# Kernel tuning notes

Measured on AMD Instinct MI355X. Metric: run time of the kernel, lower is better.

The kernel has to match this reference:

```python
import jax, jax.numpy as jnp
import numpy as np

B, NH, T, D = 2, 16, 2048, 64

def setup_inputs() -> dict:
    key = jax.random.key(0)
    kq, kk, kv = jax.random.split(key, 3)
    Q = jax.random.normal(kq, (B, NH, T, D), dtype=jnp.float32)
    K = jax.random.normal(kk, (B, NH, T, D), dtype=jnp.float32)
    V = jax.random.normal(kv, (B, NH, T, D), dtype=jnp.float32)
    return {"Q": Q, "K": K, "V": V}

def reference(Q, K, V):
    # scores: [B, nh, T, T]
    Dh = Q.shape[-1]
    scale = 1.0 / jnp.sqrt(jnp.asarray(Dh, Q.dtype))
    scores = jnp.einsum('bhtd,bhsd->bhts', Q, K) * scale
    Tq = Q.shape[2]
    causal = jnp.tril(jnp.ones((Tq, Tq), dtype=bool))
    scores = jnp.where(causal, scores, jnp.asarray(-jnp.inf, scores.dtype))
    attn = jax.nn.softmax(scores, axis=-1)
    return jnp.einsum('bhts,bhsd->bhtd', attn, V)
```

## Files before the change

kernel.cpp:

```cpp
#include <hip/hip_runtime.h>
#include <hip/hip_bf16.h>


typedef __bf16 bf16;
typedef __bf16 bf16x2 __attribute__((ext_vector_type(2)));
typedef __bf16 bf16x4 __attribute__((ext_vector_type(4)));
typedef __bf16 bf16x8 __attribute__((ext_vector_type(8)));
typedef float floatx4 __attribute__((ext_vector_type(4)));

#define T_SEQ 2048
#define DH 64
#define TKS 32
#define BHN 32
#define CEXP 0.18033688011112042f

__device__ __forceinline__ void gload16(const bf16* g, bf16* l) {
    __builtin_amdgcn_global_load_lds(
        (const __attribute__((address_space(1))) void*)g,
        (__attribute__((address_space(3))) void*)l, 16, 0, 0);
}

__global__ __launch_bounds__(256) void prep(const float* __restrict__ K,
                                            const float* __restrict__ V,
                                            bf16* __restrict__ Kb,
                                            bf16* __restrict__ Vt) {
    const int bid = (int)blockIdx.x;
    const int tid = (int)threadIdx.x;
    if (bid < 512) {
        size_t i = ((size_t)bid * 256 + tid) * 8;
        #pragma unroll
        for (int it = 0; it < 4; ++it) {
            float4 a = *(const float4*)(K + i + 0);
            float4 b = *(const float4*)(K + i + 4);
            bf16x8 o;
            o[0]=(bf16)(a.x*CEXP); o[1]=(bf16)(a.y*CEXP); o[2]=(bf16)(a.z*CEXP); o[3]=(bf16)(a.w*CEXP);
            o[4]=(bf16)(b.x*CEXP); o[5]=(bf16)(b.y*CEXP); o[6]=(bf16)(b.z*CEXP); o[7]=(bf16)(b.w*CEXP);
            *(bf16x8*)(Kb + i) = o;
            i += (size_t)512 * 256 * 8;
        }
        return;
    }
    __shared__ bf16 tile[2][64][72];
    const int vb = bid - 512;
    const int bh = vb & (BHN - 1);
    const int tp = (vb >> 5) * 128;
    #pragma unroll
    for (int tt = 0; tt < 2; ++tt) {
        const int r = tid >> 2;
        const int c = (tid & 3) * 16;
        const float* s = V + ((size_t)bh * T_SEQ + tp + tt * 64 + r) * DH + c;
        float4 f0 = *(const float4*)(s + 0);
        float4 f1 = *(const float4*)(s + 4);
        float4 f2 = *(const float4*)(s + 8);
        float4 f3 = *(const float4*)(s + 12);
        bf16x8 p0, p1;
        p0[0]=(bf16)f0.x; p0[1]=(bf16)f0.y; p0[2]=(bf16)f0.z; p0[3]=(bf16)f0.w;
        p0[4]=(bf16)f1.x; p0[5]=(bf16)f1.y; p0[6]=(bf16)f1.z; p0[7]=(bf16)f1.w;
        p1[0]=(bf16)f2.x; p1[1]=(bf16)f2.y; p1[2]=(bf16)f2.z; p1[3]=(bf16)f2.w;
        p1[4]=(bf16)f3.x; p1[5]=(bf16)f3.y; p1[6]=(bf16)f3.z; p1[7]=(bf16)f3.w;
        *(bf16x8*)&tile[tt][r][c + 0] = p0;
        *(bf16x8*)&tile[tt][r][c + 8] = p1;
    }
    __syncthreads();
    #pragma unroll
    for (int tt = 0; tt < 2; ++tt) {
        const int d   = tid >> 2;
        const int tch = (tid & 3) * 16;
        bf16x8 o0, o1;
        #pragma unroll
        for (int j = 0; j < 8; ++j) { o0[j] = tile[tt][tch + j][d]; o1[j] = tile[tt][tch + 8 + j][d]; }
        bf16* o = Vt + ((size_t)bh * DH + d) * T_SEQ + tp + tt * 64 + tch;
        *(bf16x8*)(o + 0) = o0;
        *(bf16x8*)(o + 8) = o1;
    }
}

__global__ __launch_bounds__(256, 3)
void fa_fwd(const float* __restrict__ Qg, const bf16* __restrict__ Kb,
            const bf16* __restrict__ Vt, float* __restrict__ Og)
{
    __shared__ __align__(16) bf16 smem[24576];

    const int gid   = (int)blockIdx.x;
    const int jt    = 31 - (gid >> 5);
    const int bh    = gid & (BHN - 1);

    const int tid  = (int)threadIdx.x;
    const int wave = tid >> 6;
    const int lane = tid & 63;
    const int quad = lane >> 4;
    const int l16  = lane & 15;
    const int psw  = (l16 >> 1) & 3;

    const int hf = wave >> 1;
    const int sp = wave & 1;

    const int qbaseW = jt * 64 + hf * 32;
    const int ntileW = 2 * jt + 1 + hf;
    const int c0  = (ntileW + 1) >> 1;
    const int tw0 = sp ? c0 : 0;
    const int tw1 = sp ? ntileW : c0;
    const int cnt = tw1 - tw0;

    bf16* W = smem + wave * 6144;

    const bf16* Kbh = Kb + (size_t)bh * (T_SEQ * DH);
    const bf16* Vbh = Vt + (size_t)bh * (DH * T_SEQ);
    const size_t qrb = (size_t)bh * T_SEQ;

    const int rl  = lane >> 3;
    const int kch = (lane & 7) ^ (rl & 7);
    const int vr  = lane >> 2;
    const int vch = (lane & 3) ^ ((lane >> 3) & 3);

    floatx4 oacc[4][2];
    #pragma unroll
    for (int mt = 0; mt < 4; ++mt)
        #pragma unroll
        for (int nt = 0; nt < 2; ++nt) oacc[mt][nt] = (floatx4){0.f,0.f,0.f,0.f};
    float lpart[2] = {0.f, 0.f};

    auto stageK = [&](int kt, bf16* dst) {
        const bf16* kg = Kbh + (size_t)kt * TKS * DH;
        #pragma unroll
        for (int g = 0; g < 4; ++g)
            gload16(kg + (size_t)(g * 8 + rl) * DH + kch * 8, dst + g * 512);
    };
    auto stageV = [&](int kt, bf16* dst) {
        const bf16* vg = Vbh + kt * TKS;
        #pragma unroll
        for (int g = 0; g < 4; ++g)
            gload16(vg + (size_t)(g * 16 + vr) * T_SEQ + vch * 8, dst + g * 512);
    };

    auto pk2 = [&](float a, float b) -> unsigned {
        bf16x2 h; h[0] = (bf16)a; h[1] = (bf16)b;
        return __builtin_bit_cast(unsigned, h);
    };

    if (cnt > 0) {
        bf16x8 qb[2][2];
        #pragma unroll
        for (int nt = 0; nt < 2; ++nt) {
            const int qrow = qbaseW + nt * 16 + l16;
            #pragma unroll
            for (int kk = 0; kk < 2; ++kk) {
                const float* s = Qg + (qrb + qrow) * DH + kk * 32 + quad * 8;
                float4 f0 = *(const float4*)(s);
                float4 f1 = *(const float4*)(s + 4);
                bf16x8 t;
                t[0]=(bf16)f0.x; t[1]=(bf16)f0.y; t[2]=(bf16)f0.z; t[3]=(bf16)f0.w;
                t[4]=(bf16)f1.x; t[5]=(bf16)f1.y; t[6]=(bf16)f1.z; t[7]=(bf16)f1.w;
                qb[nt][kk] = t;
            }
        }

        stageK(tw0, W);
        stageV(tw0, W + 4096);

        for (int t = tw0; t < tw1; ++t) {
            const int cur = (t - tw0) & 1;
            bf16* Kcur = W + cur * 2048;
            bf16* Vcur = W + 4096;
            const int k0 = t * TKS;

            const bool pf = (t + 1 < tw1);
            if (pf) {
                stageK(t + 1, W + (cur ^ 1) * 2048);
                __builtin_amdgcn_s_waitcnt(0x0F78);
            } else {
                __builtin_amdgcn_s_waitcnt(0x0F70);
            }

            floatx4 sa[2][2];
            #pragma unroll
            for (int mt = 0; mt < 2; ++mt)
                #pragma unroll
                for (int nt = 0; nt < 2; ++nt) sa[mt][nt] = (floatx4){0.f,0.f,0.f,0.f};
            __builtin_amdgcn_s_setprio(1);
            #pragma unroll
            for (int kk = 0; kk < 2; ++kk) {
                #pragma unroll
                for (int mt = 0; mt < 2; ++mt) {
                    bf16x8 kf = *(const bf16x8*)&Kcur[(mt * 16 + l16) * 64 + (((kk * 4 + quad) ^ (l16 & 7)) * 8)];
                    #pragma unroll
                    for (int nt = 0; nt < 2; ++nt)
                        sa[mt][nt] = __builtin_amdgcn_mfma_f32_16x16x32_bf16(kf, qb[nt][kk], sa[mt][nt], 0, 0, 0);
                }
            }
            __builtin_amdgcn_s_setprio(0);
            if (k0 + TKS - 1 > qbaseW) {
                #pragma unroll
                for (int mt = 0; mt < 2; ++mt)
                    #pragma unroll
                    for (int nt = 0; nt < 2; ++nt) {
                        const int qg = qbaseW + nt * 16 + l16;
                        #pragma unroll
                        for (int r = 0; r < 4; ++r) {
                            const int keyg = k0 + mt * 16 + quad * 4 + r;
                            if (keyg > qg) sa[mt][nt][r] = -INFINITY;
                        }
                    }
            }
            bf16x8 pfr[2];
            #pragma unroll
            for (int nt = 0; nt < 2; ++nt) {
                float p0[4], p1[4];
                #pragma unroll
                for (int r = 0; r < 4; ++r) {
                    p0[r] = __builtin_amdgcn_exp2f(sa[0][nt][r]);
                    p1[r] = __builtin_amdgcn_exp2f(sa[1][nt][r]);
                    lpart[nt] += p0[r] + p1[r];
                }
                unsigned X0 = pk2(p0[0], p0[1]);
                unsigned X1 = pk2(p0[2], p0[3]);
                unsigned Y0 = pk2(p1[0], p1[1]);
                unsigned Y1 = pk2(p1[2], p1[3]);
                asm("v_permlane32_swap_b32 %0, %1" : "+v"(X0), "+v"(Y0));
                asm("v_permlane16_swap_b32 %0, %1" : "+v"(X0), "+v"(Y0));
                asm("v_permlane32_swap_b32 %0, %1" : "+v"(X1), "+v"(Y1));
                asm("v_permlane16_swap_b32 %0, %1" : "+v"(X1), "+v"(Y1));
                uint4 u; u.x = X0; u.y = X1; u.z = Y0; u.w = Y1;
                pfr[nt] = __builtin_bit_cast(bf16x8, u);
            }
            if (pf) __builtin_amdgcn_s_waitcnt(0x0F74);
            bf16x8 vf[4];
            #pragma unroll
            for (int mt = 0; mt < 4; ++mt)
                vf[mt] = *(const bf16x8*)&Vcur[(mt * 16 + l16) * 32 + ((quad ^ psw) * 8)];
            if (pf) {
                __builtin_amdgcn_s_waitcnt(0xC07F);
                stageV(t + 1, Vcur);
            }
            __builtin_amdgcn_s_setprio(1);
            #pragma unroll
            for (int mt = 0; mt < 4; ++mt) {
                #pragma unroll
                for (int nt = 0; nt < 2; ++nt)
                    oacc[mt][nt] = __builtin_amdgcn_mfma_f32_16x16x32_bf16(vf[mt], pfr[nt], oacc[mt][nt], 0, 0, 0);
            }
            __builtin_amdgcn_s_setprio(0);
        }
    }

    __syncthreads();
    if (sp == 1) {
        bf16* a = smem + hf * 4608;
        float* al = (float*)(a + 4096);
        #pragma unroll
        for (int f = 0; f < 8; ++f) {
            bf16x4 w;
            #pragma unroll
            for (int e = 0; e < 4; ++e) w[e] = (bf16)oacc[f >> 1][f & 1][e];
            *(bf16x4*)&a[(f * 64 + lane) * 4] = w;
        }
        #pragma unroll
        for (int nt = 0; nt < 2; ++nt)
            al[nt * 64 + lane] = lpart[nt];
    }
    __syncthreads();
    if (sp == 0) {
        const bf16* a = smem + hf * 4608;
        const float* al = (const float*)(a + 4096);
        #pragma unroll
        for (int f = 0; f < 8; ++f) {
            bf16x4 w = *(const bf16x4*)&a[(f * 64 + lane) * 4];
            #pragma unroll
            for (int e = 0; e < 4; ++e) oacc[f >> 1][f & 1][e] += (float)w[e];
        }
        #pragma unroll
        for (int nt = 0; nt < 2; ++nt) lpart[nt] += al[nt * 64 + lane];

        float invl[2];
        #pragma unroll
        for (int nt = 0; nt < 2; ++nt) {
            float v = lpart[nt];
            v += __shfl_xor(v, 16);
            v += __shfl_xor(v, 32);
            invl[nt] = 1.0f / v;
        }
        #pragma unroll
        for (int nt = 0; nt < 2; ++nt) {
            const size_t qrow = qrb + qbaseW + nt * 16 + l16;
            #pragma unroll
            for (int mt = 0; mt < 4; ++mt) {
                float4 o;
                o.x = oacc[mt][nt][0] * invl[nt];
                o.y = oacc[mt][nt][1] * invl[nt];
                o.z = oacc[mt][nt][2] * invl[nt];
                o.w = oacc[mt][nt][3] * invl[nt];
                *(float4*)&Og[qrow * DH + mt * 16 + quad * 4] = o;
            }
        }
    }
}

extern "C" void kernel_launch(void* const* d_in, const int* in_sizes, int n_in,
                              void* d_out, int out_size, void* d_ws, size_t ws_size,
                              hipStream_t stream) {
    const float* Q = (const float*)d_in[0];
    const float* K = (const float*)d_in[1];
    const float* V = (const float*)d_in[2];
    float* O = (float*)d_out;
    (void)in_sizes; (void)n_in; (void)out_size; (void)ws_size;

    const size_t nelem = (size_t)BHN * T_SEQ * DH;
    bf16* Kbf = (bf16*)d_ws;
    bf16* Vtb = Kbf + nelem;

    prep<<<dim3(1024), dim3(256), 0, stream>>>(K, V, Kbf, Vtb);
    fa_fwd<<<dim3(1024), dim3(256), 0, stream>>>(Q, Kbf, Vtb, O);
}
```

Baseline: 127.6 us.

## Share K/V tiles across waves with block-wide double buffering

```diff
diff --git a/kernel.cpp b/kernel.cpp
--- a/kernel.cpp
+++ b/kernel.cpp
@@ -75,15 +75,16 @@
     }
 }
 
-__global__ __launch_bounds__(256, 3)
+__global__ __launch_bounds__(256, 4)
 void fa_fwd(const float* __restrict__ Qg, const bf16* __restrict__ Kb,
             const bf16* __restrict__ Vt, float* __restrict__ Og)
 {
-    __shared__ __align__(16) bf16 smem[24576];
-
-    const int gid   = (int)blockIdx.x;
-    const int jt    = 31 - (gid >> 5);
-    const int bh    = gid & (BHN - 1);
+    __shared__ __align__(16) bf16 smem[8192];
+
+    const int gid    = (int)blockIdx.x;
+    const int jt     = gid >> 5;
+    const int bh     = gid & (BHN - 1);
+    const int ntiles = 2 * jt + 2;
 
     const int tid  = (int)threadIdx.x;
     const int wave = tid >> 6;
@@ -92,17 +93,7 @@
     const int l16  = lane & 15;
     const int psw  = (l16 >> 1) & 3;
 
-    const int hf = wave >> 1;
-    const int sp = wave & 1;
-
-    const int qbaseW = jt * 64 + hf * 32;
-    const int ntileW = 2 * jt + 1 + hf;
-    const int c0  = (ntileW + 1) >> 1;
-    const int tw0 = sp ? c0 : 0;
-    const int tw1 = sp ? ntileW : c0;
-    const int cnt = tw1 - tw0;
-
-    bf16* W = smem + wave * 6144;
+    const int qw0 = jt * 64 + wave * 16;
 
     const bf16* Kbh = Kb + (size_t)bh * (T_SEQ * DH);
     const bf16* Vbh = Vt + (size_t)bh * (DH * T_SEQ);
@@ -112,25 +103,14 @@
     const int kch = (lane & 7) ^ (rl & 7);
     const int vr  = lane >> 2;
     const int vch = (lane & 3) ^ ((lane >> 3) & 3);
-
-    floatx4 oacc[4][2];
-    #pragma unroll
-    for (int mt = 0; mt < 4; ++mt)
-        #pragma unroll
-        for (int nt = 0; nt < 2; ++nt) oacc[mt][nt] = (floatx4){0.f,0.f,0.f,0.f};
-    float lpart[2] = {0.f, 0.f};
-
-    auto stageK = [&](int kt, bf16* dst) {
-        const bf16* kg = Kbh + (size_t)kt * TKS * DH;
-        #pragma unroll
-        for (int g = 0; g < 4; ++g)
-            gload16(kg + (size_t)(g * 8 + rl) * DH + kch * 8, dst + g * 512);
-    };
-    auto stageV = [&](int kt, bf16* dst) {
-        const bf16* vg = Vbh + kt * TKS;
-        #pragma unroll
-        for (int g = 0; g < 4; ++g)
-            gload16(vg + (size_t)(g * 16 + vr) * T_SEQ + vch * 8, dst + g * 512);
+    bf16* kdst = smem + wave * 512;
+    bf16* vdst = smem + 4096 + wave * 512;
+    const bf16* ksrc0 = Kbh + (size_t)(8 * wave + rl) * DH + kch * 8;
+    const bf16* vsrc0 = Vbh + (size_t)(16 * wave + vr) * T_SEQ + vch * 8;
+
+    auto stage = [&](int kt, int buf) {
+        gload16(ksrc0 + (size_t)kt * (TKS * DH), kdst + buf * 2048);
+        gload16(vsrc0 + kt * TKS,                vdst + buf * 2048);
     };
 
     auto pk2 = [&](float a, float b) -> unsigned {
@@ -138,160 +118,105 @@
         return __builtin_bit_cast(unsigned, h);
     };
 
-    if (cnt > 0) {
-        bf16x8 qb[2][2];
-        #pragma unroll
-        for (int nt = 0; nt < 2; ++nt) {
-            const int qrow = qbaseW + nt * 16 + l16;
-            #pragma unroll
-            for (int kk = 0; kk < 2; ++kk) {
-                const float* s = Qg + (qrb + qrow) * DH + kk * 32 + quad * 8;
-                float4 f0 = *(const float4*)(s);
-                float4 f1 = *(const float4*)(s + 4);
-                bf16x8 t;
-                t[0]=(bf16)f0.x; t[1]=(bf16)f0.y; t[2]=(bf16)f0.z; t[3]=(bf16)f0.w;
-                t[4]=(bf16)f1.x; t[5]=(bf16)f1.y; t[6]=(bf16)f1.z; t[7]=(bf16)f1.w;
-                qb[nt][kk] = t;
-            }
-        }
-
-        stageK(tw0, W);
-        stageV(tw0, W + 4096);
-
-        for (int t = tw0; t < tw1; ++t) {
-            const int cur = (t - tw0) & 1;
-            bf16* Kcur = W + cur * 2048;
-            bf16* Vcur = W + 4096;
-            const int k0 = t * TKS;
-
-            const bool pf = (t + 1 < tw1);
-            if (pf) {
-                stageK(t + 1, W + (cur ^ 1) * 2048);
-                __builtin_amdgcn_s_waitcnt(0x0F78);
-            } else {
-                __builtin_amdgcn_s_waitcnt(0x0F70);
-            }
-
-            floatx4 sa[2][2];
-            #pragma unroll
-            for (int mt = 0; mt < 2; ++mt)
-                #pragma unroll
-                for (int nt = 0; nt < 2; ++nt) sa[mt][nt] = (floatx4){0.f,0.f,0.f,0.f};
+    bf16x8 qb[2];
+    #pragma unroll
+    for (int kk = 0; kk < 2; ++kk) {
+        const float* s = Qg + (qrb + qw0 + l16) * DH + kk * 32 + quad * 8;
+        float4 f0 = *(const float4*)(s);
+        float4 f1 = *(const float4*)(s + 4);
+        bf16x8 t;
+        t[0]=(bf16)f0.x; t[1]=(bf16)f0.y; t[2]=(bf16)f0.z; t[3]=(bf16)f0.w;
+        t[4]=(bf16)f1.x; t[5]=(bf16)f1.y; t[6]=(bf16)f1.z; t[7]=(bf16)f1.w;
+        qb[kk] = t;
+    }
+
+    floatx4 oacc[4];
+    #pragma unroll
+    for (int mt = 0; mt < 4; ++mt) oacc[mt] = (floatx4){0.f,0.f,0.f,0.f};
+    float lpart = 0.f;
+    const floatx4 zf4 = {0.f, 0.f, 0.f, 0.f};
+
+    stage(0, 0);
+    __builtin_amdgcn_s_waitcnt(0x0F70);
+    __syncthreads();
+
+    for (int t = 0; t < ntiles; ++t) {
+        const int cur = t & 1;
+        const bf16* Kcur = smem + cur * 2048;
+        const bf16* Vcur = smem + 4096 + cur * 2048;
+        const int k0 = t * TKS;
+        const bool pf = (t + 1 < ntiles);
+
+        if (pf) stage(t + 1, cur ^ 1);
+
+        if (k0 <= qw0 + 15) {
+            floatx4 sa[2] = {zf4, zf4};
             __builtin_amdgcn_s_setprio(1);
             #pragma unroll
-            for (int kk = 0; kk < 2; ++kk) {
+            for (int kk = 0; kk < 2; ++kk)
                 #pragma unroll
                 for (int mt = 0; mt < 2; ++mt) {
                     bf16x8 kf = *(const bf16x8*)&Kcur[(mt * 16 + l16) * 64 + (((kk * 4 + quad) ^ (l16 & 7)) * 8)];
-                    #pragma unroll
-                    for (int nt = 0; nt < 2; ++nt)
-                        sa[mt][nt] = __builtin_amdgcn_mfma_f32_16x16x32_bf16(kf, qb[nt][kk], sa[mt][nt], 0, 0, 0);
+                    sa[mt] = __builtin_amdgcn_mfma_f32_16x16x32_bf16(kf, qb[kk], sa[mt], 0, 0, 0);
                 }
-            }
             __builtin_amdgcn_s_setprio(0);
-            if (k0 + TKS - 1 > qbaseW) {
+            if (k0 + TKS - 1 > qw0) {
+                const int qg = qw0 + l16;
                 #pragma unroll
                 for (int mt = 0; mt < 2; ++mt)
                     #pragma unroll
-                    for (int nt = 0; nt < 2; ++nt) {
-                        const int qg = qbaseW + nt * 16 + l16;
-                        #pragma unroll
-                        for (int r = 0; r < 4; ++r) {
-                            const int keyg = k0 + mt * 16 + quad * 4 + r;
-                            if (keyg > qg) sa[mt][nt][r] = -INFINITY;
-                        }
+                    for (int r = 0; r < 4; ++r) {
+                        const int keyg = k0 + mt * 16 + quad * 4 + r;
+                        if (keyg > qg) sa[mt][r] = -INFINITY;
                     }
             }
-            bf16x8 pfr[2];
-            #pragma unroll
-            for (int nt = 0; nt < 2; ++nt) {
-                float p0[4], p1[4];
-                #pragma unroll
-                for (int r = 0; r < 4; ++r) {
-                    p0[r] = __builtin_amdgcn_exp2f(sa[0][nt][r]);
-                    p1[r] = __builtin_amdgcn_exp2f(sa[1][nt][r]);
-                    lpart[nt] += p0[r] + p1[r];
-                }
-                unsigned X0 = pk2(p0[0], p0[1]);
-                unsigned X1 = pk2(p0[2], p0[3]);
-                unsigned Y0 = pk2(p1[0], p1[1]);
-                unsigned Y1 = pk2(p1[2], p1[3]);
-                asm("v_permlane32_swap_b32 %0, %1" : "+v"(X0), "+v"(Y0));
-                asm("v_permlane16_swap_b32 %0, %1" : "+v"(X0), "+v"(Y0));
-                asm("v_permlane32_swap_b32 %0, %1" : "+v"(X1), "+v"(Y1));
-                asm("v_permlane16_swap_b32 %0, %1" : "+v"(X1), "+v"(Y1));
-                uint4 u; u.x = X0; u.y = X1; u.z = Y0; u.w = Y1;
-                pfr[nt] = __builtin_bit_cast(bf16x8, u);
+            float p0[4], p1[4];
+            #pragma unroll
+            for (int r = 0; r < 4; ++r) {
+                p0[r] = __builtin_amdgcn_exp2f(sa[0][r]);
+                p1[r] = __builtin_amdgcn_exp2f(sa[1][r]);
+                lpart += p0[r] + p1[r];
             }
-            if (pf) __builtin_amdgcn_s_waitcnt(0x0F74);
+            unsigned X0 = pk2(p0[0], p0[1]);
+            unsigned X1 = pk2(p0[2], p0[3]);
+            unsigned Y0 = pk2(p1[0], p1[1]);
+            unsigned Y1 = pk2(p1[2], p1[3]);
+            asm("v_permlane32_swap_b32 %0, %1" : "+v"(X0), "+v"(Y0));
+            asm("v_permlane16_swap_b32 %0, %1" : "+v"(X0), "+v"(Y0));
+            asm("v_permlane32_swap_b32 %0, %1" : "+v"(X1), "+v"(Y1));
+            asm("v_permlane16_swap_b32 %0, %1" : "+v"(X1), "+v"(Y1));
+            uint4 u; u.x = X0; u.y = X1; u.z = Y0; u.w = Y1;
+            bf16x8 pfr = __builtin_bit_cast(bf16x8, u);
             bf16x8 vf[4];
             #pragma unroll
             for (int mt = 0; mt < 4; ++mt)
                 vf[mt] = *(const bf16x8*)&Vcur[(mt * 16 + l16) * 32 + ((quad ^ psw) * 8)];
-            if (pf) {
-                __builtin_amdgcn_s_waitcnt(0xC07F);
-                stageV(t + 1, Vcur);
-            }
             __builtin_amdgcn_s_setprio(1);
             #pragma unroll
-            for (int mt = 0; mt < 4; ++mt) {
-                #pragma unroll
-                for (int nt = 0; nt < 2; ++nt)
-                    oacc[mt][nt] = __builtin_amdgcn_mfma_f32_16x16x32_bf16(vf[mt], pfr[nt], oacc[mt][nt], 0, 0, 0);
-            }
+            for (int mt = 0; mt < 4; ++mt)
+                oacc[mt] = __builtin_amdgcn_mfma_f32_16x16x32_bf16(vf[mt], pfr, oacc[mt], 0, 0, 0);
             __builtin_amdgcn_s_setprio(0);
         }
-    }
-
-    __syncthreads();
-    if (sp == 1) {
-        bf16* a = smem + hf * 4608;
-        float* al = (float*)(a + 4096);
-        #pragma unroll
-        for (int f = 0; f < 8; ++f) {
-            bf16x4 w;
-            #pragma unroll
-            for (int e = 0; e < 4; ++e) w[e] = (bf16)oacc[f >> 1][f & 1][e];
-            *(bf16x4*)&a[(f * 64 + lane) * 4] = w;
+
+        if (pf) {
+            __builtin_amdgcn_s_waitcnt(0x0F70);
+            __syncthreads();
         }
-        #pragma unroll
-        for (int nt = 0; nt < 2; ++nt)
-            al[nt * 64 + lane] = lpart[nt];
-    }
-    __syncthreads();
-    if (sp == 0) {
-        const bf16* a = smem + hf * 4608;
-        const float* al = (const float*)(a + 4096);
-        #pragma unroll
-        for (int f = 0; f < 8; ++f) {
-            bf16x4 w = *(const bf16x4*)&a[(f * 64 + lane) * 4];
-            #pragma unroll
-            for (int e = 0; e < 4; ++e) oacc[f >> 1][f & 1][e] += (float)w[e];
-        }
-        #pragma unroll
-        for (int nt = 0; nt < 2; ++nt) lpart[nt] += al[nt * 64 + lane];
-
-        float invl[2];
-        #pragma unroll
-        for (int nt = 0; nt < 2; ++nt) {
-            float v = lpart[nt];
-            v += __shfl_xor(v, 16);
-            v += __shfl_xor(v, 32);
-            invl[nt] = 1.0f / v;
-        }
-        #pragma unroll
-        for (int nt = 0; nt < 2; ++nt) {
-            const size_t qrow = qrb + qbaseW + nt * 16 + l16;
-            #pragma unroll
-            for (int mt = 0; mt < 4; ++mt) {
-                float4 o;
-                o.x = oacc[mt][nt][0] * invl[nt];
-                o.y = oacc[mt][nt][1] * invl[nt];
-                o.z = oacc[mt][nt][2] * invl[nt];
-                o.w = oacc[mt][nt][3] * invl[nt];
-                *(float4*)&Og[qrow * DH + mt * 16 + quad * 4] = o;
-            }
-        }
+    }
+
+    float v = lpart;
+    v += __shfl_xor(v, 16);
+    v += __shfl_xor(v, 32);
+    const float invl = 1.0f / v;
+    const size_t qrow = qrb + qw0 + l16;
+    #pragma unroll
+    for (int mt = 0; mt < 4; ++mt) {
+        float4 o;
+        o.x = oacc[mt][0] * invl;
+        o.y = oacc[mt][1] * invl;
+        o.z = oacc[mt][2] * invl;
+        o.w = oacc[mt][3] * invl;
+        *(float4*)&Og[qrow * DH + mt * 16 + quad * 4] = o;
     }
 }
 
```

Result: no change. 127.7 us (+0.1%).
